# Kernel optimization log

Hardware: AMD Instinct MI355X
Metric: run time of the kernel (lower is better)

Reference implementation:

```python
import jax, jax.numpy as jnp
from jax import lax
import numpy as np

B, D, H, W = 1, 20, 96, 96
N = B * (D - 4) * H * W  # one 7x7x7 guide patch per output voxel
DN = ('NCDHW', 'OIDHW', 'NCDHW')


def _conv3(x, w, b):
    # Conv3d(1,1,kernel=3,stride=1,VALID) + bias
    y = lax.conv_general_dilated(x, w, (1, 1, 1), 'VALID', dimension_numbers=DN)
    return y + b[None, :, None, None, None]


def _guide_branch(x, w1, b1, w2, b2):
    # nn.Sequential(Conv3d, ReLU, Conv3d, ReLU): 7^3 -> 5^3 -> 3^3
    return jax.nn.relu(_conv3(jax.nn.relu(_conv3(x, w1, b1)), w2, b2))


def setup_inputs() -> dict:
    key = jax.random.key(0)
    ks = jax.random.split(key, 12)
    s = 1.0 / np.sqrt(27.0)  # torch Conv3d default init scale (fan_in = 1*3*3*3)
    return {
        'x': jax.random.normal(ks[0], (B, 1, D, H, W), jnp.float32),
        'domain_neighbor': jax.random.uniform(ks[1], (1, 1, 7, 7, 7), jnp.float32),
        'guide_im': jax.random.normal(ks[2], (N, 1, 7, 7, 7), jnp.float32),
        'w1_d': jax.random.normal(ks[3], (1, 1, 3, 3, 3), jnp.float32) * s,
        'b1_d': jax.random.normal(ks[4], (1,), jnp.float32) * s,
        'w2_d': jax.random.normal(ks[5], (1, 1, 3, 3, 3), jnp.float32) * s,
        'b2_d': jax.random.normal(ks[6], (1,), jnp.float32) * s,
        'w1_r': jax.random.normal(ks[7], (1, 1, 3, 3, 3), jnp.float32) * s,
        'b1_r': jax.random.normal(ks[8], (1,), jnp.float32) * s,
        'w2_r': jax.random.normal(ks[9], (1, 1, 3, 3, 3), jnp.float32) * s,
        'b2_r': jax.random.normal(ks[10], (1,), jnp.float32) * s,
    }


def reference(x, domain_neighbor, guide_im, w1_d, b1_d, w2_d, b2_d,
              w1_r, b1_r, w2_r, b2_r):
    Bx, _, Dx, Hx, Wx = x.shape
    # kernel-generating guide nets
    domain_kernel = _guide_branch(domain_neighbor, w1_d, b1_d, w2_d, b2_d)  # (1,1,3,3,3)
    range_kernel = _guide_branch(guide_im, w1_r, b1_r, w2_r, b2_r)          # (N,1,3,3,3)
    weights = (domain_kernel * range_kernel + 1e-10).reshape(-1, 27)        # (N,27)
    # pad H,W by 1 (depth unpadded), extract all 3x3x3 patches (feature order d,h,w)
    xp = jnp.pad(x, ((0, 0), (0, 0), (0, 0), (1, 1), (1, 1)))
    p = lax.conv_general_dilated_patches(xp, (3, 3, 3), (1, 1, 1), 'VALID',
                                         dimension_numbers=DN)  # (B,27,D-2,H,W)
    p = p[:, :, 1:-1]  # keep the D-4 center-aligned depth windows (matches mat_size)
    p = p.transpose(0, 2, 3, 4, 1).reshape(-1, 27)  # (N,27)
    out = jnp.sum(weights * p, axis=1) / jnp.sum(weights, axis=1)  # weighted local mean
    return out.reshape(Bx, 1, Dx - 4, Hx, Wx)
```

## Files before the change

### kernel.cpp

```cpp
#include <hip/hip_runtime.h>
#include <hip/hip_fp16.h>


#define NPATCH 147456
#define TPB     256
#define PPB      64
#define NBLK   (NPATCH / PPB)
#define PATCH_H 346
#define PATCH_D 173
#define NF4    5488

__global__ __launch_bounds__(128) void domain_branch_kernel(
    const float* __restrict__ dn,
    const float* __restrict__ w1, const float* __restrict__ b1,
    const float* __restrict__ w2, const float* __restrict__ b2,
    float* __restrict__ dom_out)
{
    __shared__ float s_in[344];
    __shared__ float s_c1[128];
    const int t = threadIdx.x;
    for (int idx = t; idx < 343; idx += 128) s_in[idx] = dn[idx];
    __syncthreads();
    if (t < 125) {
        const int i = t / 25, j = (t / 5) % 5, k = t % 5;
        float acc = b1[0];
        const float* base = &s_in[i * 49 + j * 7 + k];
#pragma unroll
        for (int dz = 0; dz < 3; ++dz)
#pragma unroll
            for (int dy = 0; dy < 3; ++dy)
#pragma unroll
                for (int dx = 0; dx < 3; ++dx)
                    acc = fmaf(base[dz * 49 + dy * 7 + dx], w1[dz * 9 + dy * 3 + dx], acc);
        s_c1[t] = fmaxf(acc, 0.f);
    }
    __syncthreads();
    if (t < 27) {
        const int dz = t / 9, dy = (t / 3) % 3, dx = t % 3;
        float acc = b2[0];
#pragma unroll
        for (int u = 0; u < 3; ++u)
#pragma unroll
            for (int v = 0; v < 3; ++v)
#pragma unroll
                for (int q = 0; q < 3; ++q)
                    acc = fmaf(s_c1[(dz + u) * 25 + (dy + v) * 5 + (dx + q)],
                               w2[u * 9 + v * 3 + q], acc);
        dom_out[t] = fmaxf(acc, 0.f);
    }
}

__device__ __forceinline__ float h2f_lo(unsigned int q) {
    return __half2float(__ushort_as_half((unsigned short)(q & 0xffffu)));
}
__device__ __forceinline__ float h2f_hi(unsigned int q) {
    return __half2float(__ushort_as_half((unsigned short)(q >> 16)));
}

__device__ __forceinline__ void load_row(const unsigned int* __restrict__ P, float* d,
                                         int zi, int y) {
    const int h0  = zi * 49 + y * 7;
    const int par = h0 & 1;
    const int d0  = (h0 - par) >> 1;
    unsigned int q0 = P[d0], q1 = P[d0 + 1], q2 = P[d0 + 2], q3 = P[d0 + 3];
    if (par == 0) {
        d[0] = h2f_lo(q0); d[1] = h2f_hi(q0); d[2] = h2f_lo(q1); d[3] = h2f_hi(q1);
        d[4] = h2f_lo(q2); d[5] = h2f_hi(q2); d[6] = h2f_lo(q3);
    } else {
        d[0] = h2f_hi(q0); d[1] = h2f_lo(q1); d[2] = h2f_hi(q1); d[3] = h2f_lo(q2);
        d[4] = h2f_hi(q2); d[5] = h2f_lo(q3); d[6] = h2f_hi(q3);
    }
}

template<int IB, int JB, int IE, int JE>
__device__ __forceinline__ void run_tasks(const unsigned int* __restrict__ P,
                                          const float* __restrict__ w1, float bb1,
                                          const float* __restrict__ w2,
                                          float (&a2)[3][3][3])
{
#pragma unroll
    for (int i = IB; i <= IE; ++i) {
        float rw[3][3][7];
        const int j0 = (i == IB) ? JB : 0;
        const int j1 = (i == IE) ? JE : 4;
#pragma unroll
        for (int j = j0; j <= j1; ++j) {
            if (j == j0) {
#pragma unroll
                for (int u = 0; u < 3; ++u)
#pragma unroll
                    for (int dy = 0; dy < 3; ++dy)
                        load_row(P, rw[u][(j + dy) % 3], i + u, j + dy);
            } else {
#pragma unroll
                for (int u = 0; u < 3; ++u)
                    load_row(P, rw[u][(j + 2) % 3], i + u, j + 2);
            }

            float c1r[5];
#pragma unroll
            for (int k = 0; k < 5; ++k) {
                float a = bb1;
#pragma unroll
                for (int u = 0; u < 3; ++u)
#pragma unroll
                    for (int v = 0; v < 3; ++v) {
                        const float* rr = rw[u][(j + v) % 3];
#pragma unroll
                        for (int w = 0; w < 3; ++w)
                            a = fmaf(rr[k + w], w1[u * 9 + v * 3 + w], a);
                    }
                c1r[k] = fmaxf(a, 0.f);
            }

#pragma unroll
            for (int dz2 = 0; dz2 < 3; ++dz2) {
                const int u2 = i - dz2;
                if (u2 >= 0 && u2 < 3) {
#pragma unroll
                    for (int v2 = 0; v2 < 3; ++v2) {
                        const int dy2 = j - v2;
                        if (dy2 >= 0 && dy2 < 3) {
#pragma unroll
                            for (int dx2 = 0; dx2 < 3; ++dx2)
#pragma unroll
                                for (int q = 0; q < 3; ++q)
                                    a2[dz2][dy2][dx2] =
                                        fmaf(c1r[dx2 + q],
                                             w2[u2 * 9 + v2 * 3 + q],
                                             a2[dz2][dy2][dx2]);
                        }
                    }
                }
            }
        }
    }
}

__global__ __launch_bounds__(TPB, 3) void jbf_main_kernel(
    const float* __restrict__ guide, const float* __restrict__ x,
    const float* __restrict__ w1, const float* __restrict__ b1,
    const float* __restrict__ w2, const float* __restrict__ b2,
    const float* __restrict__ dom, float* __restrict__ out)
{
    union SM {
        unsigned short tile[PPB * PATCH_H];
        float part[3][PPB][27];
    };
    __shared__ SM sm;

    const int tid  = threadIdx.x;
    const int wid  = tid >> 6;
    const int lane = tid & 63;
    const int blk  = blockIdx.x;

    const float4* __restrict__ src =
        reinterpret_cast<const float4*>(guide + (size_t)blk * (PPB * 343));

#define STORE4(IT, C) do {                                       \
        int flat = (IT) * (TPB * 4) + tid * 4;                   \
        int p    = flat / 343;                                   \
        int rs   = flat - p * 343;                               \
        int dst  = p * PATCH_H + rs;                             \
        float v4[4] = {(C).x, (C).y, (C).z, (C).w};              \
        _Pragma("unroll")                                        \
        for (int e = 0; e < 4; ++e) {                            \
            sm.tile[dst] = __half_as_ushort(__float2half(v4[e]));\
            ++dst; if (++rs == 343) { rs = 0; dst += 3; }        \
        }                                                        \
    } while (0)

    {
        float4 buf[4];
#pragma unroll
        for (int k = 0; k < 4; ++k) buf[k] = src[k * TPB + tid];

#pragma unroll 1
        for (int it0 = 0; it0 < 20; it0 += 4) {
#pragma unroll
            for (int k = 0; k < 4; ++k) {
                float4 cur = buf[k];
                int idx = (it0 + 4 + k) * TPB + tid;
                if (idx > NF4 - 1) idx = NF4 - 1;
                buf[k] = src[idx];
                STORE4(it0 + k, cur);
            }
        }
        STORE4(20, buf[0]);
        if (tid < 112) STORE4(21, buf[1]);
    }
#undef STORE4
    __syncthreads();

    const unsigned int* __restrict__ P =
        reinterpret_cast<const unsigned int*>(sm.tile) + lane * PATCH_D;
    const float bb1 = b1[0];

    float a2[3][3][3];
    {
        const float init = (wid == 0) ? b2[0] : 0.f;
#pragma unroll
        for (int a = 0; a < 3; ++a)
#pragma unroll
            for (int b = 0; b < 3; ++b)
#pragma unroll
                for (int c = 0; c < 3; ++c) a2[a][b][c] = init;
    }

    if      (wid == 0) run_tasks<0, 0, 1, 1>(P, w1, bb1, w2, a2);
    else if (wid == 1) run_tasks<1, 2, 2, 3>(P, w1, bb1, w2, a2);
    else if (wid == 2) run_tasks<2, 4, 3, 4>(P, w1, bb1, w2, a2);
    else               run_tasks<4, 0, 4, 4>(P, w1, bb1, w2, a2);

    __syncthreads();

    if (wid != 0) {
#pragma unroll
        for (int t = 0; t < 27; ++t)
            sm.part[wid - 1][lane][t] = a2[t / 9][(t / 3) % 3][t % 3];
    }
    __syncthreads();

    if (wid == 0) {
        const int n   = blk * PPB + lane;
        const int dd  = n / 9216;
        const int rem = n - dd * 9216;
        const int h   = rem / 96;
        const int w_  = rem - h * 96;

        float num = 0.f, den = 0.f;
#pragma unroll
        for (int dz = 0; dz < 3; ++dz)
#pragma unroll
            for (int dy = 0; dy < 3; ++dy)
#pragma unroll
                for (int dx = 0; dx < 3; ++dx) {
                    const int t = dz * 9 + dy * 3 + dx;
                    const float r2 = fmaxf(a2[dz][dy][dx] + sm.part[0][lane][t]
                                           + sm.part[1][lane][t]
                                           + sm.part[2][lane][t], 0.f);
                    const float wt = fmaf(dom[t], r2, 1e-10f);
                    const int yy = h - 1 + dy, xx = w_ - 1 + dx;
                    float xv = 0.f;
                    if (yy >= 0 && yy < 96 && xx >= 0 && xx < 96)
                        xv = x[(dd + 1 + dz) * 9216 + yy * 96 + xx];
                    num = fmaf(wt, xv, num);
                    den += wt;
                }
        out[n] = num / den;
    }
}

extern "C" void kernel_launch(void* const* d_in, const int* in_sizes, int n_in,
                              void* d_out, int out_size, void* d_ws, size_t ws_size,
                              hipStream_t stream) {
    const float* x     = (const float*)d_in[0];
    const float* dn    = (const float*)d_in[1];
    const float* guide = (const float*)d_in[2];
    const float* w1_d  = (const float*)d_in[3];
    const float* b1_d  = (const float*)d_in[4];
    const float* w2_d  = (const float*)d_in[5];
    const float* b2_d  = (const float*)d_in[6];
    const float* w1_r  = (const float*)d_in[7];
    const float* b1_r  = (const float*)d_in[8];
    const float* w2_r  = (const float*)d_in[9];
    const float* b2_r  = (const float*)d_in[10];
    float* out = (float*)d_out;
    float* dom = (float*)d_ws;

    domain_branch_kernel<<<1, 128, 0, stream>>>(dn, w1_d, b1_d, w2_d, b2_d, dom);
    jbf_main_kernel<<<NBLK, TPB, 0, stream>>>(guide, x, w1_r, b1_r, w2_r,
                                              b2_r, dom, out);
}
```

Measured before the change: 52.54 us.

## Make blocks persistent over three tiles with register prefetch of next guide tile

Each block now processes three consecutive 64-patch tiles instead of one, cutting the grid to 768 blocks. While computing the current tile, the block prefetches the first 12 float4 chunks of the next tile into registers, then writes them and streams the rest into shared memory after compute. The work split across the four waves changes to whole z-slices. Partial sums are exchanged in fp16 through a separate, smaller shared array, with each wave storing only the output slices it touches. This aims to overlap global loads with compute, but adds register pressure from the 12-entry prefetch buffer and precision loss on the partial sums.

```diff
diff --git a/kernel.cpp b/kernel.cpp
--- a/kernel.cpp
+++ b/kernel.cpp
@@ -5,10 +5,12 @@
 #define NPATCH 147456
 #define TPB     256
 #define PPB      64
-#define NBLK   (NPATCH / PPB)
+#define TILES     3
+#define NBLK    768
 #define PATCH_H 346
 #define PATCH_D 173
 #define NF4    5488
+#define RBUF     12
 
 __global__ __launch_bounds__(128) void domain_branch_kernel(
     const float* __restrict__ dn,
@@ -56,6 +58,12 @@
 __device__ __forceinline__ float h2f_hi(unsigned int q) {
     return __half2float(__ushort_as_half((unsigned short)(q >> 16)));
 }
+__device__ __forceinline__ float h2f(unsigned short u) {
+    return __half2float(__ushort_as_half(u));
+}
+__device__ __forceinline__ unsigned short f2h(float f) {
+    return __half_as_ushort(__float2half(f));
+}
 
 __device__ __forceinline__ void load_row(const unsigned int* __restrict__ P, float* d,
                                          int zi, int y) {
@@ -143,19 +151,13 @@
     const float* __restrict__ w2, const float* __restrict__ b2,
     const float* __restrict__ dom, float* __restrict__ out)
 {
-    union SM {
-        unsigned short tile[PPB * PATCH_H];
-        float part[3][PPB][27];
-    };
-    __shared__ SM sm;
+    __shared__ unsigned short tile[PPB * PATCH_H];
+    __shared__ unsigned short part[PPB][54];
 
     const int tid  = threadIdx.x;
     const int wid  = tid >> 6;
     const int lane = tid & 63;
-    const int blk  = blockIdx.x;
-
-    const float4* __restrict__ src =
-        reinterpret_cast<const float4*>(guide + (size_t)blk * (PPB * 343));
+    const int g0   = blockIdx.x * TILES;
 
 #define STORE4(IT, C) do {                                       \
         int flat = (IT) * (TPB * 4) + tid * 4;                   \
@@ -165,16 +167,17 @@
         float v4[4] = {(C).x, (C).y, (C).z, (C).w};              \
         _Pragma("unroll")                                        \
         for (int e = 0; e < 4; ++e) {                            \
-            sm.tile[dst] = __half_as_ushort(__float2half(v4[e]));\
+            tile[dst] = f2h(v4[e]);                              \
             ++dst; if (++rs == 343) { rs = 0; dst += 3; }        \
         }                                                        \
     } while (0)
 
     {
+        const float4* __restrict__ src =
+            reinterpret_cast<const float4*>(guide + (size_t)g0 * (PPB * 343));
         float4 buf[4];
 #pragma unroll
         for (int k = 0; k < 4; ++k) buf[k] = src[k * TPB + tid];
-
 #pragma unroll 1
         for (int it0 = 0; it0 < 20; it0 += 4) {
 #pragma unroll
@@ -189,66 +192,121 @@
         STORE4(20, buf[0]);
         if (tid < 112) STORE4(21, buf[1]);
     }
+    __syncthreads();
+
+    const float bb1 = b1[0];
+    const float bb2 = b2[0];
+
+#pragma unroll 1
+    for (int t = 0; t < TILES; ++t) {
+        const bool have_next = (t + 1 < TILES);
+        const float4* __restrict__ sn =
+            reinterpret_cast<const float4*>(guide +
+                (size_t)(g0 + t + 1) * (PPB * 343));
+
+        float4 rbuf[RBUF];
+        if (have_next) {
+#pragma unroll
+            for (int r = 0; r < RBUF; ++r) rbuf[r] = sn[r * TPB + tid];
+        }
+
+        const unsigned int* __restrict__ P =
+            reinterpret_cast<const unsigned int*>(tile) + lane * PATCH_D;
+
+        float a2[3][3][3];
+        {
+            const float init = (wid == 0) ? bb2 : 0.f;
+#pragma unroll
+            for (int a = 0; a < 3; ++a)
+#pragma unroll
+                for (int b = 0; b < 3; ++b)
+#pragma unroll
+                    for (int c = 0; c < 3; ++c) a2[a][b][c] = init;
+        }
+
+        if      (wid == 0) run_tasks<0, 0, 1, 4>(P, w1, bb1, w2, a2);
+        else if (wid == 1) run_tasks<2, 0, 2, 4>(P, w1, bb1, w2, a2);
+        else if (wid == 2) run_tasks<3, 0, 3, 4>(P, w1, bb1, w2, a2);
+        else               run_tasks<4, 0, 4, 4>(P, w1, bb1, w2, a2);
+
+        if (wid == 1) {
+#pragma unroll
+            for (int q = 0; q < 27; ++q)
+                part[lane][q] = f2h(a2[q / 9][(q / 3) % 3][q % 3]);
+        } else if (wid == 2) {
+#pragma unroll
+            for (int dz = 1; dz < 3; ++dz)
+#pragma unroll
+                for (int dy = 0; dy < 3; ++dy)
+#pragma unroll
+                    for (int dx = 0; dx < 3; ++dx)
+                        part[lane][27 + (dz - 1) * 9 + dy * 3 + dx] =
+                            f2h(a2[dz][dy][dx]);
+        } else if (wid == 3) {
+#pragma unroll
+            for (int dy = 0; dy < 3; ++dy)
+#pragma unroll
+                for (int dx = 0; dx < 3; ++dx)
+                    part[lane][45 + dy * 3 + dx] = f2h(a2[2][dy][dx]);
+        }
+        __syncthreads();
+
+        if (wid == 0) {
+            const int n   = (g0 + t) * PPB + lane;
+            const int dd  = n / 9216;
+            const int rem = n - dd * 9216;
+            const int h   = rem / 96;
+            const int w_  = rem - h * 96;
+
+            float num = 0.f, den = 0.f;
+#pragma unroll
+            for (int dz = 0; dz < 3; ++dz)
+#pragma unroll
+                for (int dy = 0; dy < 3; ++dy)
+#pragma unroll
+                    for (int dx = 0; dx < 3; ++dx) {
+                        const int q27 = dz * 9 + dy * 3 + dx;
+                        float r2 = a2[dz][dy][dx] + h2f(part[lane][q27]);
+                        if (dz >= 1)
+                            r2 += h2f(part[lane][27 + (dz - 1) * 9 + dy * 3 + dx]);
+                        if (dz == 2)
+                            r2 += h2f(part[lane][45 + dy * 3 + dx]);
+                        r2 = fmaxf(r2, 0.f);
+                        const float wt = fmaf(dom[q27], r2, 1e-10f);
+                        const int yy = h - 1 + dy, xx = w_ - 1 + dx;
+                        float xv = 0.f;
+                        if (yy >= 0 && yy < 96 && xx >= 0 && xx < 96)
+                            xv = x[(dd + 1 + dz) * 9216 + yy * 96 + xx];
+                        num = fmaf(wt, xv, num);
+                        den += wt;
+                    }
+            out[n] = num / den;
+        }
+
+        if (have_next) {
+#pragma unroll
+            for (int r = 0; r < RBUF; ++r) STORE4(r, rbuf[r]);
+
+            float4 buf2[4];
+#pragma unroll
+            for (int k = 0; k < 4; ++k) buf2[k] = sn[(RBUF + k) * TPB + tid];
+#pragma unroll 1
+            for (int it0 = RBUF; it0 + 4 <= 20; it0 += 4) {
+#pragma unroll
+                for (int k = 0; k < 4; ++k) {
+                    float4 cur = buf2[k];
+                    int idx = (it0 + 4 + k) * TPB + tid;
+                    if (idx > NF4 - 1) idx = NF4 - 1;
+                    buf2[k] = sn[idx];
+                    STORE4(it0 + k, cur);
+                }
+            }
+            STORE4(20, buf2[0]);
+            if (tid < 112) STORE4(21, buf2[1]);
+            __syncthreads();
+        }
+    }
 #undef STORE4
-    __syncthreads();
-
-    const unsigned int* __restrict__ P =
-        reinterpret_cast<const unsigned int*>(sm.tile) + lane * PATCH_D;
-    const float bb1 = b1[0];
-
-    float a2[3][3][3];
-    {
-        const float init = (wid == 0) ? b2[0] : 0.f;
-#pragma unroll
-        for (int a = 0; a < 3; ++a)
-#pragma unroll
-            for (int b = 0; b < 3; ++b)
-#pragma unroll
-                for (int c = 0; c < 3; ++c) a2[a][b][c] = init;
-    }
-
-    if      (wid == 0) run_tasks<0, 0, 1, 1>(P, w1, bb1, w2, a2);
-    else if (wid == 1) run_tasks<1, 2, 2, 3>(P, w1, bb1, w2, a2);
-    else if (wid == 2) run_tasks<2, 4, 3, 4>(P, w1, bb1, w2, a2);
-    else               run_tasks<4, 0, 4, 4>(P, w1, bb1, w2, a2);
-
-    __syncthreads();
-
-    if (wid != 0) {
-#pragma unroll
-        for (int t = 0; t < 27; ++t)
-            sm.part[wid - 1][lane][t] = a2[t / 9][(t / 3) % 3][t % 3];
-    }
-    __syncthreads();
-
-    if (wid == 0) {
-        const int n   = blk * PPB + lane;
-        const int dd  = n / 9216;
-        const int rem = n - dd * 9216;
-        const int h   = rem / 96;
-        const int w_  = rem - h * 96;
-
-        float num = 0.f, den = 0.f;
-#pragma unroll
-        for (int dz = 0; dz < 3; ++dz)
-#pragma unroll
-            for (int dy = 0; dy < 3; ++dy)
-#pragma unroll
-                for (int dx = 0; dx < 3; ++dx) {
-                    const int t = dz * 9 + dy * 3 + dx;
-                    const float r2 = fmaxf(a2[dz][dy][dx] + sm.part[0][lane][t]
-                                           + sm.part[1][lane][t]
-                                           + sm.part[2][lane][t], 0.f);
-                    const float wt = fmaf(dom[t], r2, 1e-10f);
-                    const int yy = h - 1 + dy, xx = w_ - 1 + dx;
-                    float xv = 0.f;
-                    if (yy >= 0 && yy < 96 && xx >= 0 && xx < 96)
-                        xv = x[(dd + 1 + dz) * 9216 + yy * 96 + xx];
-                    num = fmaf(wt, xv, num);
-                    den += wt;
-                }
-        out[n] = num / den;
-    }
 }
 
 extern "C" void kernel_launch(void* const* d_in, const int* in_sizes, int n_in,
```

New measurement: 93.77 us. 78.5% more time.
